# Kernel tuning notes

Hardware: AMD Instinct MI355X
Metric: run time of the kernel (lower is better)

## Reference

```python
import jax, jax.numpy as jnp
import numpy as np
import math

HIDDEN = 256
D = 256  # attention_head_size (num_heads=1)
LN_EPS = 1e-5


def setup_inputs() -> dict:
    key = jax.random.key(0)
    ks = jax.random.split(key, 12)
    b, n = 8, 256
    s = 0.02
    return {
        "hidden_states": jax.random.normal(ks[0], (b, n, HIDDEN), jnp.float32),
        "structure_matrix": jax.random.normal(ks[1], (b, n, n, D), jnp.float32),
        "Wq": jax.random.normal(ks[2], (HIDDEN, D), jnp.float32) * s,
        "bq": jnp.zeros((D,), jnp.float32),
        "Wk": jax.random.normal(ks[3], (D, D), jnp.float32) * s,
        "bk": jnp.zeros((D,), jnp.float32),
        "Wv": jax.random.normal(ks[4], (HIDDEN, D), jnp.float32) * s,
        "bv": jnp.zeros((D,), jnp.float32),
        "Wo": jax.random.normal(ks[5], (D, D), jnp.float32) * s,
        "bo": jnp.zeros((D,), jnp.float32),
        "ln_gamma": jnp.ones((D,), jnp.float32),
        "ln_beta": jnp.zeros((D,), jnp.float32),
    }


def _layer_norm(x, gamma, beta):
    mu = jnp.mean(x, axis=-1, keepdims=True)
    var = jnp.mean(jnp.square(x - mu), axis=-1, keepdims=True)
    return (x - mu) * jax.lax.rsqrt(var + LN_EPS) * gamma + beta


def reference(hidden_states, structure_matrix, Wq, bq, Wk, bk, Wv, bv, Wo, bo, ln_gamma, ln_beta):
    # projections
    q = hidden_states @ Wq + bq            # [b, n, d]
    k = structure_matrix @ Wk + bk         # [b, l, r, d]
    v = hidden_states @ Wv + bv            # [b, n, d]
    # pair-biased attention: each (l, r) pair attends over all n tokens
    scores = jnp.einsum('bnd,blrd->blrn', q, k) / math.sqrt(D)  # [b, l, r, n]
    probs = jax.nn.softmax(scores, axis=-1)  # dropout is identity in eval
    ctx = jnp.einsum('blrn,bnd->blrd', probs, v)  # [b, l, r, d]
    out = ctx @ Wo + bo
    return _layer_norm(out + structure_matrix, ln_gamma, ln_beta)
```

## Files before the change

### kernel.cpp

```cpp
#include <hip/hip_runtime.h>
#include <hip/hip_bf16.h>

typedef __attribute__((ext_vector_type(8))) short short8v;
typedef __attribute__((ext_vector_type(4))) float f32x4;
typedef __attribute__((ext_vector_type(8))) unsigned short us8;
typedef const __attribute__((address_space(1))) void* gas_t;
typedef __attribute__((address_space(3))) void* las_t;

__device__ __forceinline__ unsigned short f2bf(float f) {
  union { __hip_bfloat16 h; unsigned short u; } c;
  c.h = __float2bfloat16(f);
  return c.u;
}
__device__ __forceinline__ unsigned int f2bf2(float lo, float hi) {
  union { __hip_bfloat162 h; unsigned int u; } c;
  c.h = __float22bfloat162_rn(make_float2(lo, hi));
  return c.u;
}

__global__ __launch_bounds__(256) void make_w(
    const float* __restrict__ Wq, const float* __restrict__ Wk,
    const float* __restrict__ Wv, const float* __restrict__ Wo,
    const float* __restrict__ bq, const float* __restrict__ bk,
    const float* __restrict__ bv, float* __restrict__ WA,
    float* __restrict__ WB, float* __restrict__ wb2,
    float* __restrict__ cq, float* __restrict__ cv, float* __restrict__ cb) {
  __shared__ float wq[256], wv[256], bqs[256], bvs[256];
  const int i = blockIdx.x, t = threadIdx.x;
  wq[t] = Wq[i * 256 + t];
  wv[t] = Wv[i * 256 + t];
  bqs[t] = bq[t];
  bvs[t] = bv[t];
  __syncthreads();
  float sa = 0.f, sb = 0.f;
#pragma unroll 8
  for (int d = 0; d < 256; d++) {
    sa = fmaf(wq[d], Wk[t * 256 + d], sa);
    sb = fmaf(wv[d], Wo[d * 256 + t], sb);
  }
  WA[i * 256 + t] = sa * 0.0625f;
  WB[i * 256 + t] = sb;
  if (t == 0) {
    float s = 0.f;
#pragma unroll 8
    for (int d = 0; d < 256; d++) s = fmaf(wq[d], bk[d], s);
    wb2[i] = s * 0.0625f;
  }
  if (i == 0) {
    float s1 = 0.f, s2 = 0.f;
#pragma unroll 8
    for (int d = 0; d < 256; d++) {
      s1 = fmaf(bqs[d], Wk[t * 256 + d], s1);
      s2 = fmaf(bvs[d], Wo[d * 256 + t], s2);
    }
    cq[t] = s1 * 0.0625f;
    cv[t] = s2;
    if (t == 0) {
      float s = 0.f;
      for (int d = 0; d < 256; d++) s = fmaf(bk[d], bqs[d], s);
      cb[0] = s * 0.0625f;
    }
  }
}

__global__ __launch_bounds__(256) void bn_k(
    const float* __restrict__ hs, const float* __restrict__ wb2,
    const float* __restrict__ cb, float* __restrict__ ebn) {
  __shared__ float w2s[256];
  const int b = blockIdx.x, t = threadIdx.x;
  w2s[t] = wb2[t];
  __syncthreads();
  const float* row = hs + (size_t)(b * 256 + t) * 256;
  float s = cb[0];
#pragma unroll 8
  for (int d = 0; d < 256; d++) s = fmaf(row[d], w2s[d], s);
  ebn[b * 256 + t] = __expf(s);
}

__global__ __launch_bounds__(256) void prep2(
    const float* __restrict__ hs, const float* __restrict__ WA,
    const float* __restrict__ WB, const float* __restrict__ cq,
    const float* __restrict__ cv, const float* __restrict__ ebn,
    unsigned short* __restrict__ W2c, unsigned short* __restrict__ V2c) {
  __shared__ float rows[8][256];
  const int tid = threadIdx.x;
  const int g0 = blockIdx.x * 8;
#pragma unroll
  for (int j = 0; j < 8; j++) rows[j][tid] = hs[(size_t)(g0 + j) * 256 + tid];
  __syncthreads();
  const float cqv = cq[tid], cvv = cv[tid];
  float aq[8], av[8];
#pragma unroll
  for (int j = 0; j < 8; j++) { aq[j] = cqv; av[j] = cvv; }
#pragma unroll 8
  for (int i = 0; i < 256; i++) {
    const float wa = WA[i * 256 + tid];
    const float wb = WB[i * 256 + tid];
#pragma unroll
    for (int j = 0; j < 8; j++) {
      aq[j] = fmaf(rows[j][i], wa, aq[j]);
      av[j] = fmaf(rows[j][i], wb, av[j]);
    }
  }
  const int bb = g0 >> 8, n0 = g0 & 255;
  {
    const int kc = tid >> 5, lh = (tid >> 3) & 3, j8 = tid & 7;
    unsigned short* dst = W2c + bb * 65536 + kc * 8192 + (n0 >> 4) * 512 +
                          lh * 128 + (n0 & 15) * 8 + j8;
#pragma unroll
    for (int jj = 0; jj < 8; jj++) dst[jj * 8] = f2bf(aq[jj]);
  }
  {
    const int kc = n0 >> 5, lh = (n0 >> 3) & 3;
    us8 vp;
#pragma unroll
    for (int j = 0; j < 8; j++)
      vp[j] = f2bf(av[j] * ebn[bb * 256 + n0 + j]);
    *(us8*)(V2c + bb * 65536 + kc * 8192 + (tid >> 4) * 512 + lh * 128 +
            (tid & 15) * 8) = vp;
  }
}

__device__ __forceinline__ void stage_b(const unsigned short* src,
                                        unsigned short* lds, int lane) {
#pragma unroll
  for (int i = 0; i < 4; i++)
    __builtin_amdgcn_global_load_lds((gas_t)(src + i * 512 + lane * 8),
                                     (las_t)(lds + i * 512), 16, 0, 0);
}

__global__ __launch_bounds__(256, 3) void pair_attn11(
    const float* __restrict__ S, const float* __restrict__ bo,
    const float* __restrict__ gamma, const float* __restrict__ beta,
    const float* __restrict__ ebn, const unsigned short* __restrict__ W2c,
    const unsigned short* __restrict__ V2c, float* __restrict__ out) {
  __shared__ unsigned short sB[2][8192];
  __shared__ unsigned short sE[4096];

  const int tid = threadIdx.x;
  const int w = tid >> 6;
  const int lane = tid & 63;
  const int l16 = lane & 15;
  const int lhi = lane >> 4;
  const int bid = blockIdx.x;
  const int idx = (bid & 7) * 1024 + (bid >> 3);
  const int rblk = idx & 3;
  const int lrow = (idx >> 2) & 255;
  const int bat = idx >> 10;

  const size_t base = ((size_t)((bat * 256 + lrow) * 256 + rblk * 64)) * 256;
  const float* Srow = S + base + (size_t)(w * 16 + l16) * 256;

  short8v sf[8];
#pragma unroll
  for (int kc = 0; kc < 8; kc++) {
    const float4 u = *(const float4*)(Srow + kc * 32 + lhi * 8);
    const float4 v = *(const float4*)(Srow + kc * 32 + lhi * 8 + 4);
    us8 p;
    unsigned int* pu = (unsigned int*)&p;
    pu[0] = f2bf2(u.x, u.y);
    pu[1] = f2bf2(u.z, u.w);
    pu[2] = f2bf2(v.x, v.y);
    pu[3] = f2bf2(v.z, v.w);
    sf[kc] = *(short8v*)&p;
  }

  {
    const unsigned short eb = f2bf(ebn[bat * 256 + tid]);
    unsigned short* d0 =
        sE + (tid >> 5) * 512 + ((tid >> 3) & 3) * 128 + (tid & 7);
#pragma unroll
    for (int t = 0; t < 16; t++) d0[t * 8] = eb;
  }

  asm volatile("s_waitcnt lgkmcnt(0)" ::: "memory");
  asm volatile("s_waitcnt vmcnt(0)" ::: "memory");
  __builtin_amdgcn_sched_barrier(0);

  const unsigned short* W2b = W2c + (size_t)bat * 65536;
  const unsigned short* V2b = V2c + (size_t)bat * 65536;

  stage_b(W2b + w * 2048, &sB[0][w * 2048], lane);

  f32x4 acc[16];
#pragma unroll
  for (int t = 0; t < 16; t++) acc[t] = (f32x4){0.f, 0.f, 0.f, 0.f};

#pragma unroll
  for (int q = 0; q < 8; q++) {
    asm volatile("s_waitcnt vmcnt(0)" ::: "memory");
    __builtin_amdgcn_s_barrier();
    if (q < 7)
      stage_b(W2b + (q + 1) * 8192 + w * 2048, &sB[(q + 1) & 1][w * 2048],
              lane);
    else
      stage_b(V2b + w * 2048, &sB[0][w * 2048], lane);
    __builtin_amdgcn_sched_barrier(0);
    const unsigned short* bbuf = &sB[q & 1][0];
#pragma unroll
    for (int nt = 0; nt < 16; nt++) {
      const short8v af = *(const short8v*)(bbuf + nt * 512 + lane * 8);
      acc[nt] =
          __builtin_amdgcn_mfma_f32_16x16x32_bf16(af, sf[q], acc[nt], 0, 0, 0);
    }
  }

  unsigned int pkd[32];
#pragma unroll
  for (int nt = 0; nt < 16; nt++) {
    const float p0 = __expf(acc[nt][0]);
    const float p1 = __expf(acc[nt][1]);
    const float p2 = __expf(acc[nt][2]);
    const float p3 = __expf(acc[nt][3]);
    pkd[nt * 2] = f2bf2(p0, p1);
    pkd[nt * 2 + 1] = f2bf2(p2, p3);
  }

  const int A0 = (l16 + ((lhi & 1) * 32)) * 4;
  const int A1 = A0 + 64;
  const bool lo = (lhi < 2);

  f32x4 accE = (f32x4){0.f, 0.f, 0.f, 0.f};
#pragma unroll
  for (int t = 0; t < 16; t++) acc[t] = (f32x4){0.f, 0.f, 0.f, 0.f};

#pragma unroll
  for (int qq = 0; qq < 8; qq++) {
    asm volatile("s_waitcnt vmcnt(0)" ::: "memory");
    __builtin_amdgcn_s_barrier();
    if (qq < 7)
      stage_b(V2b + (qq + 1) * 8192 + w * 2048, &sB[(qq + 1) & 1][w * 2048],
              lane);
    __builtin_amdgcn_sched_barrier(0);
    const unsigned int e0 = __builtin_amdgcn_ds_bpermute(A0, pkd[4 * qq + 0]);
    const unsigned int o0 = __builtin_amdgcn_ds_bpermute(A0, pkd[4 * qq + 2]);
    const unsigned int e1 = __builtin_amdgcn_ds_bpermute(A0, pkd[4 * qq + 1]);
    const unsigned int o1 = __builtin_amdgcn_ds_bpermute(A0, pkd[4 * qq + 3]);
    const unsigned int e2 = __builtin_amdgcn_ds_bpermute(A1, pkd[4 * qq + 0]);
    const unsigned int o2 = __builtin_amdgcn_ds_bpermute(A1, pkd[4 * qq + 2]);
    const unsigned int e3 = __builtin_amdgcn_ds_bpermute(A1, pkd[4 * qq + 1]);
    const unsigned int o3 = __builtin_amdgcn_ds_bpermute(A1, pkd[4 * qq + 3]);
    union { unsigned int u[4]; short8v v; } bp_;
    bp_.u[0] = lo ? e0 : o0;
    bp_.u[1] = lo ? e1 : o1;
    bp_.u[2] = lo ? e2 : o2;
    bp_.u[3] = lo ? e3 : o3;
    const short8v bp = bp_.v;
    const unsigned short* bbuf = &sB[qq & 1][0];
    const short8v ae = *(const short8v*)(sE + qq * 512 + lane * 8);
    accE = __builtin_amdgcn_mfma_f32_16x16x32_bf16(ae, bp, accE, 0, 0, 0);
#pragma unroll
    for (int ct = 0; ct < 16; ct++) {
      const short8v af = *(const short8v*)(bbuf + ct * 512 + lane * 8);
      acc[ct] =
          __builtin_amdgcn_mfma_f32_16x16x32_bf16(af, bp, acc[ct], 0, 0, 0);
    }
  }
  __builtin_amdgcn_sched_barrier(0);

  const float inv = 1.f / accE[0];
  float s1 = 0.f, s2 = 0.f;
#pragma unroll
  for (int ct = 0; ct < 16; ct++) {
    const float4 rz = *(const float4*)(Srow + ct * 16 + lhi * 4);
    const float4 b4 = *(const float4*)(bo + ct * 16 + lhi * 4);
    f32x4 v;
    v[0] = acc[ct][0] * inv + b4.x + rz.x;
    v[1] = acc[ct][1] * inv + b4.y + rz.y;
    v[2] = acc[ct][2] * inv + b4.z + rz.z;
    v[3] = acc[ct][3] * inv + b4.w + rz.w;
#pragma unroll
    for (int g = 0; g < 4; g++) {
      s1 += v[g];
      s2 = fmaf(v[g], v[g], s2);
    }
    acc[ct] = v;
  }
  s1 += __shfl_xor(s1, 16); s2 += __shfl_xor(s2, 16);
  s1 += __shfl_xor(s1, 32); s2 += __shfl_xor(s2, 32);
  const float mean = s1 * (1.f / 256.f);
  const float rstd = rsqrtf(s2 * (1.f / 256.f) - mean * mean + 1e-5f);
  float* Orow = out + base + (size_t)(w * 16 + l16) * 256;
#pragma unroll
  for (int ct = 0; ct < 16; ct++) {
    const float4 g4 = *(const float4*)(gamma + ct * 16 + lhi * 4);
    const float4 be4 = *(const float4*)(beta + ct * 16 + lhi * 4);
    float4 ov;
    ov.x = (acc[ct][0] - mean) * rstd * g4.x + be4.x;
    ov.y = (acc[ct][1] - mean) * rstd * g4.y + be4.y;
    ov.z = (acc[ct][2] - mean) * rstd * g4.z + be4.z;
    ov.w = (acc[ct][3] - mean) * rstd * g4.w + be4.w;
    *(float4*)(Orow + ct * 16 + lhi * 4) = ov;
  }
}

extern "C" void kernel_launch(void* const* d_in, const int* in_sizes, int n_in,
                              void* d_out, int out_size, void* d_ws, size_t ws_size,
                              hipStream_t stream) {
  const float* hs    = (const float*)d_in[0];
  const float* S     = (const float*)d_in[1];
  const float* Wq    = (const float*)d_in[2];
  const float* bq    = (const float*)d_in[3];
  const float* Wk    = (const float*)d_in[4];
  const float* bk    = (const float*)d_in[5];
  const float* Wv    = (const float*)d_in[6];
  const float* bv    = (const float*)d_in[7];
  const float* Wo    = (const float*)d_in[8];
  const float* bo    = (const float*)d_in[9];
  const float* gamma = (const float*)d_in[10];
  const float* beta  = (const float*)d_in[11];

  unsigned short* W2c = (unsigned short*)d_ws;
  unsigned short* V2c = W2c + 8 * 256 * 256;
  float* WA  = (float*)(V2c + 8 * 256 * 256);
  float* WB  = WA + 256 * 256;
  float* wb2 = WB + 256 * 256;
  float* cq  = wb2 + 256;
  float* cv  = cq + 256;
  float* cb  = cv + 256;
  float* ebn = cb + 256;

  make_w<<<256, 256, 0, stream>>>(Wq, Wk, Wv, Wo, bq, bk, bv, WA, WB, wb2, cq,
                                  cv, cb);
  bn_k<<<8, 256, 0, stream>>>(hs, wb2, cb, ebn);
  prep2<<<256, 256, 0, stream>>>(hs, WA, WB, cq, cv, ebn, W2c, V2c);
  pair_attn11<<<8192, 256, 0, stream>>>(S, bo, gamma, beta, ebn, W2c, V2c,
                                        (float*)d_out);
}
```

Baseline: 517.2 us.

## Use 512-thread blocks with four-stage LDS ring for weight staging

Doubles the block to 8 waves covering 128 pair rows, so each staged weight chunk in LDS is shared by twice as many waves. The LDS buffer becomes a 4-deep ring with prefetch three chunks ahead, and partial vmcnt waits replace the full drains. The block-to-batch mapping also changes so consecutive blocks interleave batches. This raises LDS per block and register pressure under launch_bounds(512,4), which may lower occupancy.

```diff
diff --git a/kernel.cpp b/kernel.cpp
--- a/kernel.cpp
+++ b/kernel.cpp
@@ -121,20 +121,20 @@
   }
 }
 
-__device__ __forceinline__ void stage_b(const unsigned short* src,
-                                        unsigned short* lds, int lane) {
-#pragma unroll
-  for (int i = 0; i < 4; i++)
+__device__ __forceinline__ void stage8(const unsigned short* src,
+                                       unsigned short* lds, int lane) {
+#pragma unroll
+  for (int i = 0; i < 2; i++)
     __builtin_amdgcn_global_load_lds((gas_t)(src + i * 512 + lane * 8),
                                      (las_t)(lds + i * 512), 16, 0, 0);
 }
 
-__global__ __launch_bounds__(256, 3) void pair_attn11(
+__global__ __launch_bounds__(512, 4) void pair_attn12(
     const float* __restrict__ S, const float* __restrict__ bo,
     const float* __restrict__ gamma, const float* __restrict__ beta,
     const float* __restrict__ ebn, const unsigned short* __restrict__ W2c,
     const unsigned short* __restrict__ V2c, float* __restrict__ out) {
-  __shared__ unsigned short sB[2][8192];
+  __shared__ unsigned short sB[4][8192];
   __shared__ unsigned short sE[4096];
 
   const int tid = threadIdx.x;
@@ -143,12 +143,12 @@
   const int l16 = lane & 15;
   const int lhi = lane >> 4;
   const int bid = blockIdx.x;
-  const int idx = (bid & 7) * 1024 + (bid >> 3);
-  const int rblk = idx & 3;
-  const int lrow = (idx >> 2) & 255;
-  const int bat = idx >> 10;
-
-  const size_t base = ((size_t)((bat * 256 + lrow) * 256 + rblk * 64)) * 256;
+  const int bat = bid & 7;
+  const int idx = bid >> 3;
+  const int rblk = idx & 1;
+  const int lrow = idx >> 1;
+
+  const size_t base = ((size_t)((bat * 256 + lrow) * 256 + rblk * 128)) * 256;
   const float* Srow = S + base + (size_t)(w * 16 + l16) * 256;
 
   short8v sf[8];
@@ -165,7 +165,7 @@
     sf[kc] = *(short8v*)&p;
   }
 
-  {
+  if (tid < 256) {
     const unsigned short eb = f2bf(ebn[bat * 256 + tid]);
     unsigned short* d0 =
         sE + (tid >> 5) * 512 + ((tid >> 3) & 3) * 128 + (tid & 7);
@@ -180,7 +180,9 @@
   const unsigned short* W2b = W2c + (size_t)bat * 65536;
   const unsigned short* V2b = V2c + (size_t)bat * 65536;
 
-  stage_b(W2b + w * 2048, &sB[0][w * 2048], lane);
+  stage8(W2b + 0 * 8192 + w * 1024, &sB[0][w * 1024], lane);
+  stage8(W2b + 1 * 8192 + w * 1024, &sB[1][w * 1024], lane);
+  stage8(W2b + 2 * 8192 + w * 1024, &sB[2][w * 1024], lane);
 
   f32x4 acc[16];
 #pragma unroll
@@ -188,15 +190,16 @@
 
 #pragma unroll
   for (int q = 0; q < 8; q++) {
-    asm volatile("s_waitcnt vmcnt(0)" ::: "memory");
+    asm volatile("s_waitcnt vmcnt(4)" ::: "memory");
     __builtin_amdgcn_s_barrier();
-    if (q < 7)
-      stage_b(W2b + (q + 1) * 8192 + w * 2048, &sB[(q + 1) & 1][w * 2048],
-              lane);
-    else
-      stage_b(V2b + w * 2048, &sB[0][w * 2048], lane);
+    {
+      const int t3 = q + 3;
+      const unsigned short* src = (t3 < 8) ? (W2b + t3 * 8192)
+                                           : (V2b + (t3 - 8) * 8192);
+      stage8(src + w * 1024, &sB[t3 & 3][w * 1024], lane);
+    }
     __builtin_amdgcn_sched_barrier(0);
-    const unsigned short* bbuf = &sB[q & 1][0];
+    const unsigned short* bbuf = &sB[q & 3][0];
 #pragma unroll
     for (int nt = 0; nt < 16; nt++) {
       const short8v af = *(const short8v*)(bbuf + nt * 512 + lane * 8);
@@ -226,11 +229,17 @@
 
 #pragma unroll
   for (int qq = 0; qq < 8; qq++) {
-    asm volatile("s_waitcnt vmcnt(0)" ::: "memory");
+    if (qq < 6) {
+      asm volatile("s_waitcnt vmcnt(4)" ::: "memory");
+    } else if (qq == 6) {
+      asm volatile("s_waitcnt vmcnt(2)" ::: "memory");
+    } else {
+      asm volatile("s_waitcnt vmcnt(0)" ::: "memory");
+    }
     __builtin_amdgcn_s_barrier();
-    if (qq < 7)
-      stage_b(V2b + (qq + 1) * 8192 + w * 2048, &sB[(qq + 1) & 1][w * 2048],
-              lane);
+    if (qq < 5)
+      stage8(V2b + (qq + 3) * 8192 + w * 1024, &sB[(qq + 3) & 3][w * 1024],
+             lane);
     __builtin_amdgcn_sched_barrier(0);
     const unsigned int e0 = __builtin_amdgcn_ds_bpermute(A0, pkd[4 * qq + 0]);
     const unsigned int o0 = __builtin_amdgcn_ds_bpermute(A0, pkd[4 * qq + 2]);
@@ -246,7 +255,7 @@
     bp_.u[2] = lo ? e2 : o2;
     bp_.u[3] = lo ? e3 : o3;
     const short8v bp = bp_.v;
-    const unsigned short* bbuf = &sB[qq & 1][0];
+    const unsigned short* bbuf = &sB[qq & 3][0];
     const short8v ae = *(const short8v*)(sE + qq * 512 + lane * 8);
     accE = __builtin_amdgcn_mfma_f32_16x16x32_bf16(ae, bp, accE, 0, 0, 0);
 #pragma unroll
@@ -324,6 +333,6 @@
                                   cv, cb);
   bn_k<<<8, 256, 0, stream>>>(hs, wb2, cb, ebn);
   prep2<<<256, 256, 0, stream>>>(hs, WA, WB, cq, cv, ebn, W2c, V2c);
-  pair_attn11<<<8192, 256, 0, stream>>>(S, bo, gamma, beta, ebn, W2c, V2c,
+  pair_attn12<<<4096, 512, 0, stream>>>(S, bo, gamma, beta, ebn, W2c, V2c,
                                         (float*)d_out);
 }
```

After: 608.4 us. 17.6% more time.

## Deepen LDS staging to four buffers with a unified prefetch pipeline

Applied to the files above, without the earlier changes.

Merges the score and context MFMA loops into one 16-step loop that prefetches B tiles three stages ahead into a quad-buffered LDS ring. Partial vmcnt waits replace full drains, and s_setprio raises priority around the MFMA bursts. The goal is to hide global-to-LDS latency, including at the switch from the score phase to the context phase. LDS use doubles and launch bounds drop from 3 to 2 blocks per CU, so occupancy may fall.

```diff
diff --git a/kernel.cpp b/kernel.cpp
--- a/kernel.cpp
+++ b/kernel.cpp
@@ -129,12 +129,12 @@
                                      (las_t)(lds + i * 512), 16, 0, 0);
 }
 
-__global__ __launch_bounds__(256, 3) void pair_attn11(
+__global__ __launch_bounds__(256, 2) void pair_attn13(
     const float* __restrict__ S, const float* __restrict__ bo,
     const float* __restrict__ gamma, const float* __restrict__ beta,
     const float* __restrict__ ebn, const unsigned short* __restrict__ W2c,
     const unsigned short* __restrict__ V2c, float* __restrict__ out) {
-  __shared__ unsigned short sB[2][8192];
+  __shared__ unsigned short sB[4][8192];
   __shared__ unsigned short sE[4096];
 
   const int tid = threadIdx.x;
@@ -180,80 +180,86 @@
   const unsigned short* W2b = W2c + (size_t)bat * 65536;
   const unsigned short* V2b = V2c + (size_t)bat * 65536;
 
-  stage_b(W2b + w * 2048, &sB[0][w * 2048], lane);
+  stage_b(W2b + 0 * 8192 + w * 2048, &sB[0][w * 2048], lane);
+  stage_b(W2b + 1 * 8192 + w * 2048, &sB[1][w * 2048], lane);
+  stage_b(W2b + 2 * 8192 + w * 2048, &sB[2][w * 2048], lane);
 
   f32x4 acc[16];
+  f32x4 accE = (f32x4){0.f, 0.f, 0.f, 0.f};
+  unsigned int pkd[32];
 #pragma unroll
   for (int t = 0; t < 16; t++) acc[t] = (f32x4){0.f, 0.f, 0.f, 0.f};
-
-#pragma unroll
-  for (int q = 0; q < 8; q++) {
-    asm volatile("s_waitcnt vmcnt(0)" ::: "memory");
-    __builtin_amdgcn_s_barrier();
-    if (q < 7)
-      stage_b(W2b + (q + 1) * 8192 + w * 2048, &sB[(q + 1) & 1][w * 2048],
-              lane);
-    else
-      stage_b(V2b + w * 2048, &sB[0][w * 2048], lane);
-    __builtin_amdgcn_sched_barrier(0);
-    const unsigned short* bbuf = &sB[q & 1][0];
-#pragma unroll
-    for (int nt = 0; nt < 16; nt++) {
-      const short8v af = *(const short8v*)(bbuf + nt * 512 + lane * 8);
-      acc[nt] =
-          __builtin_amdgcn_mfma_f32_16x16x32_bf16(af, sf[q], acc[nt], 0, 0, 0);
-    }
-  }
-
-  unsigned int pkd[32];
-#pragma unroll
-  for (int nt = 0; nt < 16; nt++) {
-    const float p0 = __expf(acc[nt][0]);
-    const float p1 = __expf(acc[nt][1]);
-    const float p2 = __expf(acc[nt][2]);
-    const float p3 = __expf(acc[nt][3]);
-    pkd[nt * 2] = f2bf2(p0, p1);
-    pkd[nt * 2 + 1] = f2bf2(p2, p3);
-  }
 
   const int A0 = (l16 + ((lhi & 1) * 32)) * 4;
   const int A1 = A0 + 64;
   const bool lo = (lhi < 2);
 
-  f32x4 accE = (f32x4){0.f, 0.f, 0.f, 0.f};
-#pragma unroll
-  for (int t = 0; t < 16; t++) acc[t] = (f32x4){0.f, 0.f, 0.f, 0.f};
-
-#pragma unroll
-  for (int qq = 0; qq < 8; qq++) {
-    asm volatile("s_waitcnt vmcnt(0)" ::: "memory");
+#pragma unroll
+  for (int t = 0; t < 16; t++) {
+    if (t < 14) {
+      asm volatile("s_waitcnt vmcnt(8)" ::: "memory");
+    } else if (t == 14) {
+      asm volatile("s_waitcnt vmcnt(4)" ::: "memory");
+    } else {
+      asm volatile("s_waitcnt vmcnt(0)" ::: "memory");
+    }
     __builtin_amdgcn_s_barrier();
-    if (qq < 7)
-      stage_b(V2b + (qq + 1) * 8192 + w * 2048, &sB[(qq + 1) & 1][w * 2048],
-              lane);
+    if (t + 3 < 16) {
+      const int t3 = t + 3;
+      const unsigned short* src =
+          (t3 < 8) ? (W2b + t3 * 8192) : (V2b + (t3 - 8) * 8192);
+      stage_b(src + w * 2048, &sB[t3 & 3][w * 2048], lane);
+    }
     __builtin_amdgcn_sched_barrier(0);
-    const unsigned int e0 = __builtin_amdgcn_ds_bpermute(A0, pkd[4 * qq + 0]);
-    const unsigned int o0 = __builtin_amdgcn_ds_bpermute(A0, pkd[4 * qq + 2]);
-    const unsigned int e1 = __builtin_amdgcn_ds_bpermute(A0, pkd[4 * qq + 1]);
-    const unsigned int o1 = __builtin_amdgcn_ds_bpermute(A0, pkd[4 * qq + 3]);
-    const unsigned int e2 = __builtin_amdgcn_ds_bpermute(A1, pkd[4 * qq + 0]);
-    const unsigned int o2 = __builtin_amdgcn_ds_bpermute(A1, pkd[4 * qq + 2]);
-    const unsigned int e3 = __builtin_amdgcn_ds_bpermute(A1, pkd[4 * qq + 1]);
-    const unsigned int o3 = __builtin_amdgcn_ds_bpermute(A1, pkd[4 * qq + 3]);
-    union { unsigned int u[4]; short8v v; } bp_;
-    bp_.u[0] = lo ? e0 : o0;
-    bp_.u[1] = lo ? e1 : o1;
-    bp_.u[2] = lo ? e2 : o2;
-    bp_.u[3] = lo ? e3 : o3;
-    const short8v bp = bp_.v;
-    const unsigned short* bbuf = &sB[qq & 1][0];
-    const short8v ae = *(const short8v*)(sE + qq * 512 + lane * 8);
-    accE = __builtin_amdgcn_mfma_f32_16x16x32_bf16(ae, bp, accE, 0, 0, 0);
-#pragma unroll
-    for (int ct = 0; ct < 16; ct++) {
-      const short8v af = *(const short8v*)(bbuf + ct * 512 + lane * 8);
-      acc[ct] =
-          __builtin_amdgcn_mfma_f32_16x16x32_bf16(af, bp, acc[ct], 0, 0, 0);
+    const unsigned short* bbuf = &sB[t & 3][0];
+
+    if (t < 8) {
+      __builtin_amdgcn_s_setprio(1);
+#pragma unroll
+      for (int nt = 0; nt < 16; nt++) {
+        const short8v af = *(const short8v*)(bbuf + nt * 512 + lane * 8);
+        acc[nt] = __builtin_amdgcn_mfma_f32_16x16x32_bf16(af, sf[t], acc[nt],
+                                                          0, 0, 0);
+      }
+      __builtin_amdgcn_s_setprio(0);
+      if (t == 7) {
+#pragma unroll
+        for (int nt = 0; nt < 16; nt++) {
+          const float p0 = __expf(acc[nt][0]);
+          const float p1 = __expf(acc[nt][1]);
+          const float p2 = __expf(acc[nt][2]);
+          const float p3 = __expf(acc[nt][3]);
+          pkd[nt * 2] = f2bf2(p0, p1);
+          pkd[nt * 2 + 1] = f2bf2(p2, p3);
+          acc[nt] = (f32x4){0.f, 0.f, 0.f, 0.f};
+        }
+      }
+    } else {
+      const int qq = t - 8;
+      const unsigned int e0 = __builtin_amdgcn_ds_bpermute(A0, pkd[4 * qq + 0]);
+      const unsigned int o0 = __builtin_amdgcn_ds_bpermute(A0, pkd[4 * qq + 2]);
+      const unsigned int e1 = __builtin_amdgcn_ds_bpermute(A0, pkd[4 * qq + 1]);
+      const unsigned int o1 = __builtin_amdgcn_ds_bpermute(A0, pkd[4 * qq + 3]);
+      const unsigned int e2 = __builtin_amdgcn_ds_bpermute(A1, pkd[4 * qq + 0]);
+      const unsigned int o2 = __builtin_amdgcn_ds_bpermute(A1, pkd[4 * qq + 2]);
+      const unsigned int e3 = __builtin_amdgcn_ds_bpermute(A1, pkd[4 * qq + 1]);
+      const unsigned int o3 = __builtin_amdgcn_ds_bpermute(A1, pkd[4 * qq + 3]);
+      union { unsigned int u[4]; short8v v; } bp_;
+      bp_.u[0] = lo ? e0 : o0;
+      bp_.u[1] = lo ? e1 : o1;
+      bp_.u[2] = lo ? e2 : o2;
+      bp_.u[3] = lo ? e3 : o3;
+      const short8v bp = bp_.v;
+      const short8v ae = *(const short8v*)(sE + qq * 512 + lane * 8);
+      __builtin_amdgcn_s_setprio(1);
+      accE = __builtin_amdgcn_mfma_f32_16x16x32_bf16(ae, bp, accE, 0, 0, 0);
+#pragma unroll
+      for (int ct = 0; ct < 16; ct++) {
+        const short8v af = *(const short8v*)(bbuf + ct * 512 + lane * 8);
+        acc[ct] =
+            __builtin_amdgcn_mfma_f32_16x16x32_bf16(af, bp, acc[ct], 0, 0, 0);
+      }
+      __builtin_amdgcn_s_setprio(0);
     }
   }
   __builtin_amdgcn_sched_barrier(0);
@@ -324,6 +330,6 @@
                                   cv, cb);
   bn_k<<<8, 256, 0, stream>>>(hs, wb2, cb, ebn);
   prep2<<<256, 256, 0, stream>>>(hs, WA, WB, cq, cv, ebn, W2c, V2c);
-  pair_attn11<<<8192, 256, 0, stream>>>(S, bo, gamma, beta, ebn, W2c, V2c,
+  pair_attn13<<<8192, 256, 0, stream>>>(S, bo, gamma, beta, ebn, W2c, V2c,
                                         (float*)d_out);
 }
```

New measurement: 556.8 us. 1.08x slower.
